# Kernel optimization log

Measured on AMD Instinct MI355X. Metric: run time of the kernel, lower is better.

## Reference

```python
import jax, jax.numpy as jnp
import numpy as np

B, T, M, H = 64, 256, 512, 256  # batch, seq_len, d_model, lstm hidden


def setup_inputs() -> dict:
    key = jax.random.key(0)
    ks = jax.random.split(key, 10)
    s = 0.05  # weight init scale
    return {
        "enc_inputs": jax.random.normal(ks[0], (B, T, M), jnp.float32),
        "y": jax.random.normal(ks[1], (B, T, 1), jnp.float32),
        "Wd_w": jax.random.normal(ks[2], (M, 2 * H), jnp.float32) * s,  # W_d: Linear(2H, M)
        "Wd_b": jnp.zeros((M,), jnp.float32),
        "Ud_w": jax.random.normal(ks[3], (M, M), jnp.float32) * s,      # U_d: Linear(M, M, bias=False)
        "vd_w": jax.random.normal(ks[4], (1, M), jnp.float32) * s,      # v_d: Linear(M, 1, bias=False)
        "wt_w": jax.random.normal(ks[5], (1, M + 1), jnp.float32) * s,  # w_tilda: Linear(M+1, 1)
        "wt_b": jnp.zeros((1,), jnp.float32),
        "Wih": jax.random.normal(ks[6], (4 * H, 1), jnp.float32) * s,   # LSTMCell input weights
        "Whh": jax.random.normal(ks[7], (4 * H, H), jnp.float32) * s,   # LSTMCell hidden weights
        "bih": jnp.zeros((4 * H,), jnp.float32),
        "bhh": jnp.zeros((4 * H,), jnp.float32),
    }


def reference(enc_inputs, y, Wd_w, Wd_b, Ud_w, vd_w, wt_w, wt_b, Wih, Whh, bih, bhh):
    # U_d(enc_inputs) is loop-invariant -> hoist (same math as recomputing each step)
    y1 = jnp.einsum('btm,nm->btn', enc_inputs, Ud_w)  # [B,T,M]

    def step(carry, y_t):
        d, s = carry  # d = h_{t-1} [B,H], s = c'_{t-1} [B,H]
        x1 = jnp.concatenate([d, s], axis=1) @ Wd_w.T + Wd_b          # [B,M]
        z1 = jnp.tanh(x1[:, None, :] + y1)                            # [B,T,M]
        l_it = jnp.einsum('btm,m->bt', z1, vd_w[0])                   # [B,T]
        beta = jax.nn.softmax(l_it, axis=1)                           # softmax over encoder steps
        c_t = jnp.einsum('bt,btm->bm', beta, enc_inputs)              # [B,M]
        y_tilda = jnp.concatenate([c_t, y_t], axis=1) @ wt_w.T + wt_b # [B,1]
        # torch LSTMCell: gate order i, f, g, o
        gates = y_tilda @ Wih.T + bih + d @ Whh.T + bhh               # [B,4H]
        i, f, g, o = jnp.split(gates, 4, axis=1)
        s_new = jax.nn.sigmoid(f) * s + jax.nn.sigmoid(i) * jnp.tanh(g)
        d_new = jax.nn.sigmoid(o) * jnp.tanh(s_new)
        return (d_new, s_new), c_t

    b = enc_inputs.shape[0]
    init = (jnp.zeros((b, H), enc_inputs.dtype), jnp.zeros((b, H), enc_inputs.dtype))
    _, cs = jax.lax.scan(step, init, jnp.swapaxes(y, 0, 1))  # cs: [T,B,M]
    return jnp.sum(cs, axis=0)  # tgt = sum_t c_t, [B,M]
```

## Files before the change

### kernel.cpp

```cpp
#include <hip/hip_runtime.h>

typedef unsigned short u16;
typedef unsigned int u32;
typedef __attribute__((ext_vector_type(8))) short short8v;
typedef __attribute__((ext_vector_type(4))) float f32x4;
typedef __attribute__((ext_vector_type(4))) unsigned int u32x4;
typedef __attribute__((ext_vector_type(2))) _Float16 f16x2;

#define NB 64
#define NT 256
#define NM 512
#define NH 256

#define K2 2.8853900817779268f
#define LOG2E 1.4426950408889634f

__device__ __forceinline__ float bf2f(u16 u) {
  union { unsigned i; float f; } c; c.i = ((unsigned)u) << 16; return c.f;
}
__device__ __forceinline__ u16 f2bf(float f) {
  union { float fv; unsigned i; } c; c.fv = f;
  unsigned i = c.i;
  return (u16)((i + 0x7fffu + ((i >> 16) & 1u)) >> 16);
}
__device__ __forceinline__ float bits2f(u32 u) {
  union { unsigned i; float f; } c; c.i = u; return c.f;
}
__device__ __forceinline__ f16x2 u2h2(u32 u) {
  union { u32 i; f16x2 h; } c; c.i = u; return c.h;
}
__device__ __forceinline__ u32 pkrtz(float a, float b) {
  auto h = __builtin_amdgcn_cvt_pkrtz(a, b);
  union { decltype(h) v; u32 i; } c; c.v = h; return c.i;
}
__device__ __forceinline__ float unpk(u32 v, int hi) {
  f16x2 h = u2h2(v);
  return hi ? (float)h.y : (float)h.x;
}
#if __has_builtin(__builtin_amdgcn_fdot2)
__device__ __forceinline__ float FDOT2(f16x2 a, f16x2 b, float c) {
  return __builtin_amdgcn_fdot2(a, b, c, false);
}
#else
__device__ __forceinline__ float FDOT2(f16x2 a, f16x2 b, float c) {
  c = fmaf((float)a.x, (float)b.x, c);
  return fmaf((float)a.y, (float)b.y, c);
}
#endif
__device__ __forceinline__ float tanh_fast(float x) {
  return 1.0f - 2.0f * __builtin_amdgcn_rcpf(1.0f + __builtin_amdgcn_exp2f(K2 * x));
}
__device__ __forceinline__ float sigmoid_fast(float x) {
  return __builtin_amdgcn_rcpf(1.0f + __builtin_amdgcn_exp2f(-LOG2E * x));
}

__global__ void convert_f32_bf16(const float* __restrict__ in, u16* __restrict__ out, int n) {
  int i = blockIdx.x * blockDim.x + threadIdx.x;
  if (i < n) out[i] = f2bf(in[i]);
}

__global__ __launch_bounds__(256) void pack_wd2(const float* __restrict__ in,
                                                u32* __restrict__ out) {
  int i = blockIdx.x * 256 + threadIdx.x;
  int k2 = i >> 9, m = i & 511;
  out[i] = pkrtz(in[m * 512 + 2 * k2], in[m * 512 + 2 * k2 + 1]);
}
__global__ __launch_bounds__(256) void pack_whh2(const float* __restrict__ in,
                                                 u32* __restrict__ out) {
  int i = blockIdx.x * 256 + threadIdx.x;
  int k2 = i >> 10, r = i & 1023;
  out[i] = pkrtz(in[r * 256 + 2 * k2], in[r * 256 + 2 * k2 + 1]);
}

__global__ __launch_bounds__(256) void gemm_y1(const u16* __restrict__ A,
                                               const u16* __restrict__ Bm,
                                               u16* __restrict__ C) {
  const int w = threadIdx.x >> 6;
  const int l = threadIdx.x & 63;
  const int kg = l >> 4;
  const int r16 = l & 15;
  const int rowbase = blockIdx.x * 64 + w * 16;
  const int colbase = blockIdx.y * 64;
  const u16* ap = A + (size_t)(rowbase + r16) * 512 + kg * 8;
  f32x4 acc0 = {0,0,0,0}, acc1 = {0,0,0,0}, acc2 = {0,0,0,0}, acc3 = {0,0,0,0};
  for (int k = 0; k < 512; k += 32) {
    short8v af = *(const short8v*)(ap + k);
    const u16* bp = Bm + (size_t)(colbase + r16) * 512 + kg * 8 + k;
    short8v b0 = *(const short8v*)(bp);
    short8v b1 = *(const short8v*)(bp + 16 * 512);
    short8v b2 = *(const short8v*)(bp + 32 * 512);
    short8v b3 = *(const short8v*)(bp + 48 * 512);
    acc0 = __builtin_amdgcn_mfma_f32_16x16x32_bf16(af, b0, acc0, 0, 0, 0);
    acc1 = __builtin_amdgcn_mfma_f32_16x16x32_bf16(af, b1, acc1, 0, 0, 0);
    acc2 = __builtin_amdgcn_mfma_f32_16x16x32_bf16(af, b2, acc2, 0, 0, 0);
    acc3 = __builtin_amdgcn_mfma_f32_16x16x32_bf16(af, b3, acc3, 0, 0, 0);
  }
  #pragma unroll
  for (int j = 0; j < 4; ++j) {
    int r = rowbase + (l >> 4) * 4 + j;
    C[(size_t)r * 512 + colbase +  0 + r16] = f2bf(K2 * acc0[j]);
    C[(size_t)r * 512 + colbase + 16 + r16] = f2bf(K2 * acc1[j]);
    C[(size_t)r * 512 + colbase + 32 + r16] = f2bf(K2 * acc2[j]);
    C[(size_t)r * 512 + colbase + 48 + r16] = f2bf(K2 * acc3[j]);
  }
}

__global__ __launch_bounds__(256) void wenc_kernel(const u16* __restrict__ encbf,
                                                   const float* __restrict__ wtw,
                                                   float* __restrict__ gwenc) {
  int b = blockIdx.x, te = threadIdx.x;
  const u16* ep = encbf + ((size_t)(b * NT + te)) * NM;
  float a = 0.0f;
  for (int c8 = 0; c8 < 64; ++c8) {
    short8v v = *(const short8v*)(ep + c8 * 8);
    #pragma unroll
    for (int jj = 0; jj < 8; ++jj) a = fmaf(bf2f((u16)v[jj]), wtw[c8 * 8 + jj], a);
  }
  gwenc[b * NT + te] = a;
}

__global__ __launch_bounds__(512) void bsum_kernel(const u16* __restrict__ encbf,
                                                   const float* __restrict__ gbeta,
                                                   float* __restrict__ out) {
  __shared__ float bl[NT];
  int b = blockIdx.x, m = threadIdx.x;
  if (m < 256) bl[m] = gbeta[b * NT + m];
  __syncthreads();
  const u16* ep = encbf + (size_t)b * NT * NM + m;
  float a = 0.0f;
  #pragma unroll 8
  for (int te = 0; te < NT; ++te)
    a = fmaf(bf2f(ep[(size_t)te * NM]), bl[te], a);
  out[b * NM + m] = a;
}

__global__ void __launch_bounds__(1024) attn_scan(
    const u16* __restrict__ y1bf,
    const u32* __restrict__ wdt2,
    const u32* __restrict__ whht2,
    const float* __restrict__ Wd_b,
    const float* __restrict__ vd,
    const float* __restrict__ wtw,
    const float* __restrict__ wtb,
    const float* __restrict__ Wih,
    const float* __restrict__ bih,
    const float* __restrict__ bhh,
    const float* __restrict__ yin,
    const float* __restrict__ gwenc,
    float* __restrict__ gbeta)
{
  extern __shared__ char ldsraw[];
  u32* gph    = (u32*)ldsraw;
  u32* x1ph   = (u32*)(ldsraw + 16384);
  float* gact = (float*)(ldsraw + 24576);

  __shared__ float x1_l2[NM];
  __shared__ u32 pk_ds[256];
  __shared__ float l_sl[NT];
  __shared__ float wih_l[1024];
  __shared__ float bb_l[1024];
  __shared__ float wenc_l[NT];
  __shared__ float yin_l[NT];
  __shared__ float wdb_l[NM];

  const int tid = threadIdx.x;
  const int b = blockIdx.x;
  const int w = tid >> 6, l = tid & 63;

  wih_l[tid] = Wih[tid];
  bb_l[tid] = bih[tid] + bhh[tid];
  if (tid < 256) {
    wenc_l[tid] = gwenc[b * NT + tid];
    yin_l[tid] = yin[b * NT + tid];
  }
  if (tid < 512) {
    float wb = Wd_b[tid];
    wdb_l[tid] = wb;
    x1_l2[(tid & 7) * 64 + (tid >> 3)] = K2 * wb;
  }
  for (int i = tid; i < 4096; i += 1024) gph[i] = 0;

  float vr[8];
  #pragma unroll
  for (int j = 0; j < 8; ++j) vr[j] = vd[l * 8 + j];
  float sv = 0.0f;
  #pragma unroll
  for (int j = 0; j < 8; ++j) sv += vr[j];
  #pragma unroll
  for (int off = 32; off > 0; off >>= 1) sv += __shfl_xor(sv, off, 64);
  const float Svd = sv;
  const float wtw512 = wtw[NM];
  const float wtb0 = wtb[0];

  const u16* ybase = y1bf + ((size_t)(b * NT + w * 16) << 9) + l * 8;

  float s_reg = 0.0f;
  float bacc = 0.0f;
  __syncthreads();

  #pragma unroll 1
  for (int t = 0; t < NT; ++t) {
    {
      float xr[8];
      #pragma unroll
      for (int j = 0; j < 8; ++j) xr[j] = x1_l2[j * 64 + l];
      float lout = 0.0f;
      #pragma unroll
      for (int i = 0; i < 16; ++i) {
        const int ii = (i + t) & 15;
        u32x4 V = *(const u32x4*)(ybase + ((size_t)ii << 9));
        float a = 0.0f;
        #pragma unroll
        for (int n = 0; n < 4; ++n) {
          u32 v = V[n];
          float e0 = __builtin_amdgcn_exp2f(xr[2 * n] + bits2f(v << 16));
          a = fmaf(vr[2 * n], __builtin_amdgcn_rcpf(1.0f + e0), a);
          float e1 = __builtin_amdgcn_exp2f(xr[2 * n + 1] + bits2f(v & 0xffff0000u));
          a = fmaf(vr[2 * n + 1], __builtin_amdgcn_rcpf(1.0f + e1), a);
        }
        #pragma unroll
        for (int off = 32; off > 0; off >>= 1) a += __shfl_xor(a, off, 64);
        if (l == ii) lout = Svd - 2.0f * a;
      }
      if (l < 16) l_sl[w * 16 + l] = lout;
    }
    __syncthreads();

    float yt, rden, e0, e1, e2, e3;
    {
      float v0 = l_sl[l], v1 = l_sl[64 + l], v2 = l_sl[128 + l], v3 = l_sl[192 + l];
      float mx = fmaxf(fmaxf(v0, v1), fmaxf(v2, v3));
      #pragma unroll
      for (int off = 32; off > 0; off >>= 1) mx = fmaxf(mx, __shfl_xor(mx, off, 64));
      e0 = __builtin_amdgcn_exp2f((v0 - mx) * LOG2E);
      e1 = __builtin_amdgcn_exp2f((v1 - mx) * LOG2E);
      e2 = __builtin_amdgcn_exp2f((v2 - mx) * LOG2E);
      e3 = __builtin_amdgcn_exp2f((v3 - mx) * LOG2E);
      float sq = (e0 + e1) + (e2 + e3);
      float nq = fmaf(e0, wenc_l[l], fmaf(e1, wenc_l[64 + l],
                 fmaf(e2, wenc_l[128 + l], e3 * wenc_l[192 + l])));
      #pragma unroll
      for (int off = 32; off > 0; off >>= 1) {
        sq += __shfl_xor(sq, off, 64);
        nq += __shfl_xor(nq, off, 64);
      }
      rden = __builtin_amdgcn_rcpf(sq);
      yt = nq * rden + wtw512 * yin_l[t] + wtb0;
    }
    if (w >= 4 && w < 8) {
      float e_own = (w == 4) ? e0 : (w == 5) ? e1 : (w == 6) ? e2 : e3;
      bacc = fmaf(e_own, rden, bacc);
    }

    {
      int r = tid, hb = r >> 1, sel = r & 1;
      float g = 0.0f;
      #pragma unroll
      for (int s = 0; s < 8; ++s) g += unpk(gph[s * 512 + hb], sel);
      float pre = g + yt * wih_l[r] + bb_l[r];
      float act = (r >= 512 && r < 768) ? tanh_fast(pre) : sigmoid_fast(pre);
      gact[r] = act;
    }
    __syncthreads();

    if (tid < 256) {
      int h = tid, hb = h >> 1, sel = h & 1;
      float gi = gact[h];
      float gf = gact[256 + h];
      float gg = gact[512 + h];
      float go = gact[768 + h];
      float sn = gf * s_reg + gi * gg;
      s_reg = sn;
      float dn = go * tanh_fast(sn);
      float dn1 = __shfl_xor(dn, 1, 64);
      float sn1 = __shfl_xor(sn, 1, 64);
      if (sel == 0) {
        pk_ds[hb] = pkrtz(dn, dn1);
        pk_ds[128 + hb] = pkrtz(sn, sn1);
      }
    }
    __syncthreads();

    if (w < 8) {
      float a0 = 0, a1 = 0, a2 = 0, a3 = 0, a4 = 0, a5 = 0, a6 = 0, a7 = 0;
      const u32* base = wdt2 + (size_t)(w * 32) * 512 + l * 8;
      const u32* pk = (const u32*)pk_ds + w * 32;
      #pragma unroll 8
      for (int kk = 0; kk < 32; ++kk) {
        u32x4 W0 = *(const u32x4*)(base + (size_t)kk * 512);
        u32x4 W1 = *(const u32x4*)(base + (size_t)kk * 512 + 4);
        f16x2 dk = u2h2(pk[kk]);
        a0 = FDOT2(u2h2(W0[0]), dk, a0);
        a1 = FDOT2(u2h2(W0[1]), dk, a1);
        a2 = FDOT2(u2h2(W0[2]), dk, a2);
        a3 = FDOT2(u2h2(W0[3]), dk, a3);
        a4 = FDOT2(u2h2(W1[0]), dk, a4);
        a5 = FDOT2(u2h2(W1[1]), dk, a5);
        a6 = FDOT2(u2h2(W1[2]), dk, a6);
        a7 = FDOT2(u2h2(W1[3]), dk, a7);
      }
      u32* dst = x1ph + w * 256 + l * 4;
      dst[0] = pkrtz(a0, a1);
      dst[1] = pkrtz(a2, a3);
      dst[2] = pkrtz(a4, a5);
      dst[3] = pkrtz(a6, a7);
    } else {
      const int sl = w - 8;
      float a0 = 0, a1 = 0, a2 = 0, a3 = 0, a4 = 0, a5 = 0, a6 = 0, a7 = 0;
      float c0 = 0, c1 = 0, c2 = 0, c3 = 0, c4 = 0, c5 = 0, c6 = 0, c7 = 0;
      const u32* base = whht2 + (size_t)(sl * 16) * 1024 + l * 8;
      const u32* pk = (const u32*)pk_ds + sl * 16;
      #pragma unroll 4
      for (int kk = 0; kk < 16; ++kk) {
        u32x4 Wa0 = *(const u32x4*)(base + (size_t)kk * 1024);
        u32x4 Wa1 = *(const u32x4*)(base + (size_t)kk * 1024 + 4);
        u32x4 Wc0 = *(const u32x4*)(base + (size_t)kk * 1024 + 512);
        u32x4 Wc1 = *(const u32x4*)(base + (size_t)kk * 1024 + 516);
        f16x2 dk = u2h2(pk[kk]);
        a0 = FDOT2(u2h2(Wa0[0]), dk, a0);
        a1 = FDOT2(u2h2(Wa0[1]), dk, a1);
        a2 = FDOT2(u2h2(Wa0[2]), dk, a2);
        a3 = FDOT2(u2h2(Wa0[3]), dk, a3);
        a4 = FDOT2(u2h2(Wa1[0]), dk, a4);
        a5 = FDOT2(u2h2(Wa1[1]), dk, a5);
        a6 = FDOT2(u2h2(Wa1[2]), dk, a6);
        a7 = FDOT2(u2h2(Wa1[3]), dk, a7);
        c0 = FDOT2(u2h2(Wc0[0]), dk, c0);
        c1 = FDOT2(u2h2(Wc0[1]), dk, c1);
        c2 = FDOT2(u2h2(Wc0[2]), dk, c2);
        c3 = FDOT2(u2h2(Wc0[3]), dk, c3);
        c4 = FDOT2(u2h2(Wc1[0]), dk, c4);
        c5 = FDOT2(u2h2(Wc1[1]), dk, c5);
        c6 = FDOT2(u2h2(Wc1[2]), dk, c6);
        c7 = FDOT2(u2h2(Wc1[3]), dk, c7);
      }
      u32* dst = gph + sl * 512 + l * 4;
      dst[0] = pkrtz(a0, a1);
      dst[1] = pkrtz(a2, a3);
      dst[2] = pkrtz(a4, a5);
      dst[3] = pkrtz(a6, a7);
      u32* dst2 = gph + sl * 512 + 256 + l * 4;
      dst2[0] = pkrtz(c0, c1);
      dst2[1] = pkrtz(c2, c3);
      dst2[2] = pkrtz(c4, c5);
      dst2[3] = pkrtz(c6, c7);
    }
    __syncthreads();

    if (tid < 512) {
      int m = tid, mb = m >> 1, sel = m & 1;
      float s = 0.0f;
      #pragma unroll
      for (int sI = 0; sI < 8; ++sI) s += unpk(x1ph[sI * 256 + mb], sel);
      x1_l2[(m & 7) * 64 + (m >> 3)] = K2 * (wdb_l[m] + s);
    }
    __syncthreads();
  }

  if (w >= 4 && w < 8) gbeta[b * NT + (w - 4) * 64 + l] = bacc;
}

extern "C" void kernel_launch(void* const* d_in, const int* in_sizes, int n_in,
                              void* d_out, int out_size, void* d_ws, size_t ws_size,
                              hipStream_t stream) {
  const float* enc  = (const float*)d_in[0];
  const float* yin  = (const float*)d_in[1];
  const float* Wd_w = (const float*)d_in[2];
  const float* Wd_b = (const float*)d_in[3];
  const float* Ud_w = (const float*)d_in[4];
  const float* vd_w = (const float*)d_in[5];
  const float* wt_w = (const float*)d_in[6];
  const float* wt_b = (const float*)d_in[7];
  const float* Wih  = (const float*)d_in[8];
  const float* Whh  = (const float*)d_in[9];
  const float* bih  = (const float*)d_in[10];
  const float* bhh  = (const float*)d_in[11];

  char* ws = (char*)d_ws;
  u16*   y1bf   = (u16*)(ws);
  u16*   encbf  = (u16*)(ws + 16777216);
  u16*   udbf   = (u16*)(ws + 33554432);
  u32*   wdt2   = (u32*)(ws + 34078720);
  u32*   whht2  = (u32*)(ws + 34603008);
  float* gwenc  = (float*)(ws + 35127296);
  float* gbeta  = (float*)(ws + 35192832);

  convert_f32_bf16<<<8388608 / 256, 256, 0, stream>>>(enc, encbf, 8388608);
  convert_f32_bf16<<<262144 / 256, 256, 0, stream>>>(Ud_w, udbf, 262144);
  pack_wd2<<<512, 256, 0, stream>>>(Wd_w, wdt2);
  pack_whh2<<<512, 256, 0, stream>>>(Whh, whht2);
  gemm_y1<<<dim3(256, 8), 256, 0, stream>>>(encbf, udbf, y1bf);
  wenc_kernel<<<64, 256, 0, stream>>>(encbf, wt_w, gwenc);

  hipFuncSetAttribute((const void*)attn_scan,
                      hipFuncAttributeMaxDynamicSharedMemorySize, 28672);
  attn_scan<<<64, 1024, 28672, stream>>>(y1bf, wdt2, whht2, Wd_b, vd_w,
                                         wt_w, wt_b, Wih, bih, bhh, yin, gwenc,
                                         gbeta);
  bsum_kernel<<<64, 512, 0, stream>>>(encbf, gbeta, (float*)d_out);
}
```

Baseline: 4.676 ms.

## Process two batch elements per workgroup in the attention scan, sharing weight loads

Each 1024-thread workgroup now handles two batch rows, with half the workgroup per row in the attention/softmax/LSTM-cell phases. In the matvec phases every wave loads each Whh/Wd weight vector once and applies it to both rows' hidden states, halving weight traffic per row. The grid drops from 64 to 32 workgroups and LDS use roughly doubles. Each wave now handles 32 encoder steps instead of 16, so per-step attention work per workgroup doubles and the serial critical path may lengthen.

```diff
diff --git a/kernel.cpp b/kernel.cpp
--- a/kernel.cpp
+++ b/kernel.cpp
@@ -151,34 +151,40 @@
 {
   extern __shared__ char ldsraw[];
   u32* gph    = (u32*)ldsraw;
-  u32* x1ph   = (u32*)(ldsraw + 16384);
-  float* gact = (float*)(ldsraw + 24576);
-
-  __shared__ float x1_l2[NM];
-  __shared__ u32 pk_ds[256];
-  __shared__ float l_sl[NT];
+  u32* x1ph   = (u32*)(ldsraw + 32768);
+  float* gact = (float*)(ldsraw + 49152);
+
+  __shared__ float x1_l2[2][NM];
+  __shared__ u32 pk_ds[2][256];
+  __shared__ float l_sl[2][NT];
   __shared__ float wih_l[1024];
   __shared__ float bb_l[1024];
-  __shared__ float wenc_l[NT];
-  __shared__ float yin_l[NT];
+  __shared__ float wenc_l[2][NT];
+  __shared__ float yin_l[2][NT];
   __shared__ float wdb_l[NM];
 
   const int tid = threadIdx.x;
-  const int b = blockIdx.x;
+  const int bA = blockIdx.x * 2;
   const int w = tid >> 6, l = tid & 63;
+  const int half = w >> 3;
+  const int wh = w & 7;
+  const int myb = bA + half;
 
   wih_l[tid] = Wih[tid];
   bb_l[tid] = bih[tid] + bhh[tid];
-  if (tid < 256) {
-    wenc_l[tid] = gwenc[b * NT + tid];
-    yin_l[tid] = yin[b * NT + tid];
+  if (tid < 512) {
+    int bb = tid >> 8, te = tid & 255;
+    wenc_l[bb][te] = gwenc[(bA + bb) * NT + te];
+    yin_l[bb][te] = yin[(bA + bb) * NT + te];
   }
   if (tid < 512) {
     float wb = Wd_b[tid];
     wdb_l[tid] = wb;
-    x1_l2[(tid & 7) * 64 + (tid >> 3)] = K2 * wb;
-  }
-  for (int i = tid; i < 4096; i += 1024) gph[i] = 0;
+    float v = K2 * wb;
+    x1_l2[0][(tid & 7) * 64 + (tid >> 3)] = v;
+    x1_l2[1][(tid & 7) * 64 + (tid >> 3)] = v;
+  }
+  for (int i = tid; i < 8192; i += 1024) gph[i] = 0;
 
   float vr[8];
   #pragma unroll
@@ -192,7 +198,7 @@
   const float wtw512 = wtw[NM];
   const float wtb0 = wtb[0];
 
-  const u16* ybase = y1bf + ((size_t)(b * NT + w * 16) << 9) + l * 8;
+  const u16* ybase = y1bf + ((size_t)(myb * NT + wh * 32) << 9) + l * 8;
 
   float s_reg = 0.0f;
   float bacc = 0.0f;
@@ -203,11 +209,11 @@
     {
       float xr[8];
       #pragma unroll
-      for (int j = 0; j < 8; ++j) xr[j] = x1_l2[j * 64 + l];
+      for (int j = 0; j < 8; ++j) xr[j] = x1_l2[half][j * 64 + l];
       float lout = 0.0f;
       #pragma unroll
-      for (int i = 0; i < 16; ++i) {
-        const int ii = (i + t) & 15;
+      for (int i = 0; i < 32; ++i) {
+        const int ii = (i + t) & 31;
         u32x4 V = *(const u32x4*)(ybase + ((size_t)ii << 9));
         float a = 0.0f;
         #pragma unroll
@@ -222,13 +228,14 @@
         for (int off = 32; off > 0; off >>= 1) a += __shfl_xor(a, off, 64);
         if (l == ii) lout = Svd - 2.0f * a;
       }
-      if (l < 16) l_sl[w * 16 + l] = lout;
+      if (l < 32) l_sl[half][wh * 32 + l] = lout;
     }
     __syncthreads();
 
     float yt, rden, e0, e1, e2, e3;
     {
-      float v0 = l_sl[l], v1 = l_sl[64 + l], v2 = l_sl[128 + l], v3 = l_sl[192 + l];
+      const float* ls = l_sl[half];
+      float v0 = ls[l], v1 = ls[64 + l], v2 = ls[128 + l], v3 = ls[192 + l];
       float mx = fmaxf(fmaxf(v0, v1), fmaxf(v2, v3));
       #pragma unroll
       for (int off = 32; off > 0; off >>= 1) mx = fmaxf(mx, __shfl_xor(mx, off, 64));
@@ -237,127 +244,124 @@
       e2 = __builtin_amdgcn_exp2f((v2 - mx) * LOG2E);
       e3 = __builtin_amdgcn_exp2f((v3 - mx) * LOG2E);
       float sq = (e0 + e1) + (e2 + e3);
-      float nq = fmaf(e0, wenc_l[l], fmaf(e1, wenc_l[64 + l],
-                 fmaf(e2, wenc_l[128 + l], e3 * wenc_l[192 + l])));
+      float nq = fmaf(e0, wenc_l[half][l], fmaf(e1, wenc_l[half][64 + l],
+                 fmaf(e2, wenc_l[half][128 + l], e3 * wenc_l[half][192 + l])));
       #pragma unroll
       for (int off = 32; off > 0; off >>= 1) {
         sq += __shfl_xor(sq, off, 64);
         nq += __shfl_xor(nq, off, 64);
       }
       rden = __builtin_amdgcn_rcpf(sq);
-      yt = nq * rden + wtw512 * yin_l[t] + wtb0;
-    }
-    if (w >= 4 && w < 8) {
-      float e_own = (w == 4) ? e0 : (w == 5) ? e1 : (w == 6) ? e2 : e3;
+      yt = nq * rden + wtw512 * yin_l[half][t] + wtb0;
+    }
+    if (wh >= 4) {
+      float e_own = (wh == 4) ? e0 : (wh == 5) ? e1 : (wh == 6) ? e2 : e3;
       bacc = fmaf(e_own, rden, bacc);
     }
 
     {
-      int r = tid, hb = r >> 1, sel = r & 1;
-      float g = 0.0f;
-      #pragma unroll
-      for (int s = 0; s < 8; ++s) g += unpk(gph[s * 512 + hb], sel);
-      float pre = g + yt * wih_l[r] + bb_l[r];
-      float act = (r >= 512 && r < 768) ? tanh_fast(pre) : sigmoid_fast(pre);
-      gact[r] = act;
+      int r0 = tid & 511;
+      const u32* gb = gph + half * 4096;
+      int hb0 = r0 >> 1, sel0 = r0 & 1;
+      int r1 = r0 + 512;
+      int hb1 = r1 >> 1, sel1 = r1 & 1;
+      float g0 = 0.0f, g1 = 0.0f;
+      #pragma unroll
+      for (int s = 0; s < 8; ++s) {
+        g0 += unpk(gb[s * 512 + hb0], sel0);
+        g1 += unpk(gb[s * 512 + hb1], sel1);
+      }
+      float pre0 = g0 + yt * wih_l[r0] + bb_l[r0];
+      float pre1 = g1 + yt * wih_l[r1] + bb_l[r1];
+      gact[half * 1024 + r0] = sigmoid_fast(pre0);
+      gact[half * 1024 + r1] = (r0 < 256) ? tanh_fast(pre1) : sigmoid_fast(pre1);
     }
     __syncthreads();
 
-    if (tid < 256) {
-      int h = tid, hb = h >> 1, sel = h & 1;
-      float gi = gact[h];
-      float gf = gact[256 + h];
-      float gg = gact[512 + h];
-      float go = gact[768 + h];
+    if ((tid & 511) < 256) {
+      int h = tid & 255;
+      const float* ga = gact + half * 1024;
+      float gi = ga[h];
+      float gf = ga[256 + h];
+      float gg = ga[512 + h];
+      float go = ga[768 + h];
       float sn = gf * s_reg + gi * gg;
       s_reg = sn;
       float dn = go * tanh_fast(sn);
       float dn1 = __shfl_xor(dn, 1, 64);
       float sn1 = __shfl_xor(sn, 1, 64);
-      if (sel == 0) {
-        pk_ds[hb] = pkrtz(dn, dn1);
-        pk_ds[128 + hb] = pkrtz(sn, sn1);
+      if ((h & 1) == 0) {
+        int hb = h >> 1;
+        pk_ds[half][hb] = pkrtz(dn, dn1);
+        pk_ds[half][128 + hb] = pkrtz(sn, sn1);
       }
     }
     __syncthreads();
 
-    if (w < 8) {
-      float a0 = 0, a1 = 0, a2 = 0, a3 = 0, a4 = 0, a5 = 0, a6 = 0, a7 = 0;
-      const u32* base = wdt2 + (size_t)(w * 32) * 512 + l * 8;
-      const u32* pk = (const u32*)pk_ds + w * 32;
+    {
+      float a0=0,a1=0,a2=0,a3=0,a4=0,a5=0,a6=0,a7=0;
+      float b0=0,b1=0,b2=0,b3=0,b4=0,b5=0,b6=0,b7=0;
+      const u32* base = whht2 + (size_t)(wh * 16) * 1024 + half * 512 + l * 8;
+      const u32* pkA = pk_ds[0] + wh * 16;
+      const u32* pkB = pk_ds[1] + wh * 16;
+      #pragma unroll 4
+      for (int kk = 0; kk < 16; ++kk) {
+        u32x4 W0 = *(const u32x4*)(base + (size_t)kk * 1024);
+        u32x4 W1 = *(const u32x4*)(base + (size_t)kk * 1024 + 4);
+        f16x2 dkA = u2h2(pkA[kk]);
+        f16x2 dkB = u2h2(pkB[kk]);
+        a0 = FDOT2(u2h2(W0[0]), dkA, a0);  b0 = FDOT2(u2h2(W0[0]), dkB, b0);
+        a1 = FDOT2(u2h2(W0[1]), dkA, a1);  b1 = FDOT2(u2h2(W0[1]), dkB, b1);
+        a2 = FDOT2(u2h2(W0[2]), dkA, a2);  b2 = FDOT2(u2h2(W0[2]), dkB, b2);
+        a3 = FDOT2(u2h2(W0[3]), dkA, a3);  b3 = FDOT2(u2h2(W0[3]), dkB, b3);
+        a4 = FDOT2(u2h2(W1[0]), dkA, a4);  b4 = FDOT2(u2h2(W1[0]), dkB, b4);
+        a5 = FDOT2(u2h2(W1[1]), dkA, a5);  b5 = FDOT2(u2h2(W1[1]), dkB, b5);
+        a6 = FDOT2(u2h2(W1[2]), dkA, a6);  b6 = FDOT2(u2h2(W1[2]), dkB, b6);
+        a7 = FDOT2(u2h2(W1[3]), dkA, a7);  b7 = FDOT2(u2h2(W1[3]), dkB, b7);
+      }
+      u32* dA = gph + wh * 512 + half * 256 + l * 4;
+      dA[0] = pkrtz(a0, a1); dA[1] = pkrtz(a2, a3);
+      dA[2] = pkrtz(a4, a5); dA[3] = pkrtz(a6, a7);
+      u32* dB = gph + 4096 + wh * 512 + half * 256 + l * 4;
+      dB[0] = pkrtz(b0, b1); dB[1] = pkrtz(b2, b3);
+      dB[2] = pkrtz(b4, b5); dB[3] = pkrtz(b6, b7);
+    }
+    {
+      float a0=0,a1=0,a2=0,a3=0;
+      float b0=0,b1=0,b2=0,b3=0;
+      const u32* base = wdt2 + (size_t)(wh * 32) * 512 + half * 256 + l * 4;
+      const u32* pkA = pk_ds[0] + wh * 32;
+      const u32* pkB = pk_ds[1] + wh * 32;
       #pragma unroll 8
       for (int kk = 0; kk < 32; ++kk) {
-        u32x4 W0 = *(const u32x4*)(base + (size_t)kk * 512);
-        u32x4 W1 = *(const u32x4*)(base + (size_t)kk * 512 + 4);
-        f16x2 dk = u2h2(pk[kk]);
-        a0 = FDOT2(u2h2(W0[0]), dk, a0);
-        a1 = FDOT2(u2h2(W0[1]), dk, a1);
-        a2 = FDOT2(u2h2(W0[2]), dk, a2);
-        a3 = FDOT2(u2h2(W0[3]), dk, a3);
-        a4 = FDOT2(u2h2(W1[0]), dk, a4);
-        a5 = FDOT2(u2h2(W1[1]), dk, a5);
-        a6 = FDOT2(u2h2(W1[2]), dk, a6);
-        a7 = FDOT2(u2h2(W1[3]), dk, a7);
-      }
-      u32* dst = x1ph + w * 256 + l * 4;
-      dst[0] = pkrtz(a0, a1);
-      dst[1] = pkrtz(a2, a3);
-      dst[2] = pkrtz(a4, a5);
-      dst[3] = pkrtz(a6, a7);
-    } else {
-      const int sl = w - 8;
-      float a0 = 0, a1 = 0, a2 = 0, a3 = 0, a4 = 0, a5 = 0, a6 = 0, a7 = 0;
-      float c0 = 0, c1 = 0, c2 = 0, c3 = 0, c4 = 0, c5 = 0, c6 = 0, c7 = 0;
-      const u32* base = whht2 + (size_t)(sl * 16) * 1024 + l * 8;
-      const u32* pk = (const u32*)pk_ds + sl * 16;
-      #pragma unroll 4
-      for (int kk = 0; kk < 16; ++kk) {
-        u32x4 Wa0 = *(const u32x4*)(base + (size_t)kk * 1024);
-        u32x4 Wa1 = *(const u32x4*)(base + (size_t)kk * 1024 + 4);
-        u32x4 Wc0 = *(const u32x4*)(base + (size_t)kk * 1024 + 512);
-        u32x4 Wc1 = *(const u32x4*)(base + (size_t)kk * 1024 + 516);
-        f16x2 dk = u2h2(pk[kk]);
-        a0 = FDOT2(u2h2(Wa0[0]), dk, a0);
-        a1 = FDOT2(u2h2(Wa0[1]), dk, a1);
-        a2 = FDOT2(u2h2(Wa0[2]), dk, a2);
-        a3 = FDOT2(u2h2(Wa0[3]), dk, a3);
-        a4 = FDOT2(u2h2(Wa1[0]), dk, a4);
-        a5 = FDOT2(u2h2(Wa1[1]), dk, a5);
-        a6 = FDOT2(u2h2(Wa1[2]), dk, a6);
-        a7 = FDOT2(u2h2(Wa1[3]), dk, a7);
-        c0 = FDOT2(u2h2(Wc0[0]), dk, c0);
-        c1 = FDOT2(u2h2(Wc0[1]), dk, c1);
-        c2 = FDOT2(u2h2(Wc0[2]), dk, c2);
-        c3 = FDOT2(u2h2(Wc0[3]), dk, c3);
-        c4 = FDOT2(u2h2(Wc1[0]), dk, c4);
-        c5 = FDOT2(u2h2(Wc1[1]), dk, c5);
-        c6 = FDOT2(u2h2(Wc1[2]), dk, c6);
-        c7 = FDOT2(u2h2(Wc1[3]), dk, c7);
-      }
-      u32* dst = gph + sl * 512 + l * 4;
-      dst[0] = pkrtz(a0, a1);
-      dst[1] = pkrtz(a2, a3);
-      dst[2] = pkrtz(a4, a5);
-      dst[3] = pkrtz(a6, a7);
-      u32* dst2 = gph + sl * 512 + 256 + l * 4;
-      dst2[0] = pkrtz(c0, c1);
-      dst2[1] = pkrtz(c2, c3);
-      dst2[2] = pkrtz(c4, c5);
-      dst2[3] = pkrtz(c6, c7);
+        u32x4 W = *(const u32x4*)(base + (size_t)kk * 512);
+        f16x2 dkA = u2h2(pkA[kk]);
+        f16x2 dkB = u2h2(pkB[kk]);
+        a0 = FDOT2(u2h2(W[0]), dkA, a0);  b0 = FDOT2(u2h2(W[0]), dkB, b0);
+        a1 = FDOT2(u2h2(W[1]), dkA, a1);  b1 = FDOT2(u2h2(W[1]), dkB, b1);
+        a2 = FDOT2(u2h2(W[2]), dkA, a2);  b2 = FDOT2(u2h2(W[2]), dkB, b2);
+        a3 = FDOT2(u2h2(W[3]), dkA, a3);  b3 = FDOT2(u2h2(W[3]), dkB, b3);
+      }
+      u32* dA = x1ph + wh * 256 + half * 128 + l * 2;
+      dA[0] = pkrtz(a0, a1); dA[1] = pkrtz(a2, a3);
+      u32* dB = x1ph + 2048 + wh * 256 + half * 128 + l * 2;
+      dB[0] = pkrtz(b0, b1); dB[1] = pkrtz(b2, b3);
     }
     __syncthreads();
 
-    if (tid < 512) {
-      int m = tid, mb = m >> 1, sel = m & 1;
+    {
+      int bb = tid >> 9, m = tid & 511;
+      int mb = m >> 1, sel = m & 1;
+      const u32* xp = x1ph + bb * 2048;
       float s = 0.0f;
       #pragma unroll
-      for (int sI = 0; sI < 8; ++sI) s += unpk(x1ph[sI * 256 + mb], sel);
-      x1_l2[(m & 7) * 64 + (m >> 3)] = K2 * (wdb_l[m] + s);
+      for (int sI = 0; sI < 8; ++sI) s += unpk(xp[sI * 256 + mb], sel);
+      x1_l2[bb][(m & 7) * 64 + (m >> 3)] = K2 * (wdb_l[m] + s);
     }
     __syncthreads();
   }
 
-  if (w >= 4 && w < 8) gbeta[b * NT + (w - 4) * 64 + l] = bacc;
+  if (wh >= 4) gbeta[myb * NT + (wh - 4) * 64 + l] = bacc;
 }
 
 extern "C" void kernel_launch(void* const* d_in, const int* in_sizes, int n_in,
@@ -393,8 +397,8 @@
   wenc_kernel<<<64, 256, 0, stream>>>(encbf, wt_w, gwenc);
 
   hipFuncSetAttribute((const void*)attn_scan,
-                      hipFuncAttributeMaxDynamicSharedMemorySize, 28672);
-  attn_scan<<<64, 1024, 28672, stream>>>(y1bf, wdt2, whht2, Wd_b, vd_w,
+                      hipFuncAttributeMaxDynamicSharedMemorySize, 57344);
+  attn_scan<<<32, 1024, 57344, stream>>>(y1bf, wdt2, whht2, Wd_b, vd_w,
                                          wt_w, wt_b, Wih, bih, bhh, yin, gwenc,
                                          gbeta);
   bsum_kernel<<<64, 512, 0, stream>>>(encbf, gbeta, (float*)d_out);
```

Measured after the change: 7.163 ms. 53.2% more time.
